# Kernel tuning notes

Measured on AMD Instinct MI355X. Metric: run time of the kernel, lower is better.

Reference implementation:

```python
import jax, jax.numpy as jnp
import numpy as np

N = 50000
E = 800000
C_IN, C_HID, C_OUT = 512, 128, 2
HEADS2 = 3
NEG_SLOPE = 0.2


def gat_conv(x, src, dst, W, att_src, att_dst, bias, heads, ch, concat):
    """PyG GATConv (eval mode) on pre-augmented (self-loop included) edge lists.
    x: [N, F_in], W: [F_in, heads*ch], att_*: [heads, ch], bias: [heads*ch] or [ch].
    """
    n = x.shape[0]
    h = (x @ W).reshape(n, heads, ch)                 # [N, H, C]
    a_src = (h * att_src).sum(-1)                     # [N, H]
    a_dst = (h * att_dst).sum(-1)                     # [N, H]
    e = jax.nn.leaky_relu(a_src[src] + a_dst[dst], NEG_SLOPE)  # [E', H]
    # segment softmax over edges sharing a destination node
    m = jax.ops.segment_max(e, dst, num_segments=n)
    m = jnp.where(jnp.isfinite(m), m, 0.0)
    ex = jnp.exp(e - m[dst])
    denom = jax.ops.segment_sum(ex, dst, num_segments=n)
    alpha = ex / (denom[dst] + 1e-16)                 # [E', H]
    out = jax.ops.segment_sum(h[src] * alpha[:, :, None], dst, num_segments=n)  # [N, H, C]
    out = out.reshape(n, heads * ch) if concat else out.mean(axis=1)
    return out + bias


def setup_inputs() -> dict:
    key = jax.random.key(0)
    ks = jax.random.split(key, 12)
    x = jax.random.normal(ks[0], (N, C_IN), dtype=jnp.float32)
    edge_index = jax.random.randint(ks[1], (2, E), 0, N, dtype=jnp.int64)
    s1 = 1.0 / np.sqrt(C_IN)
    s2 = 1.0 / np.sqrt(C_HID)
    return {
        "x": x,
        "edge_index": edge_index,
        "W1": jax.random.normal(ks[2], (C_IN, C_HID), dtype=jnp.float32) * s1,
        "att_src1": jax.random.normal(ks[3], (1, C_HID), dtype=jnp.float32) * s2,
        "att_dst1": jax.random.normal(ks[4], (1, C_HID), dtype=jnp.float32) * s2,
        "bias1": jnp.zeros((C_HID,), dtype=jnp.float32),
        "W2": jax.random.normal(ks[5], (C_HID, HEADS2 * C_OUT), dtype=jnp.float32) * s2,
        "att_src2": jax.random.normal(ks[6], (HEADS2, C_OUT), dtype=jnp.float32) * 0.5,
        "att_dst2": jax.random.normal(ks[7], (HEADS2, C_OUT), dtype=jnp.float32) * 0.5,
        "bias2": jnp.zeros((C_OUT,), dtype=jnp.float32),
    }


def reference(x, edge_index, W1, att_src1, att_dst1, bias1, W2, att_src2, att_dst2, bias2):
    n = x.shape[0]
    loop = jnp.arange(n, dtype=edge_index.dtype)
    src = jnp.concatenate([edge_index[0], loop])      # PyG add_self_loops=True
    dst = jnp.concatenate([edge_index[1], loop])
    h = gat_conv(x, src, dst, W1, att_src1, att_dst1, bias1, 1, C_HID, True)
    h = jax.nn.relu(h)                                # Dropout is identity in eval
    out = gat_conv(h, src, dst, W2, att_src2, att_dst2, bias2, HEADS2, C_OUT, False)
    return out
```

## Files before the change

### kernel.cpp

```cpp
#include <hip/hip_runtime.h>

#define N_NODES 50000
#define N_EDGES 800000
#define E_TOT   850000
#define C_IN    512
#define C_HID   128
#define NEG     0.2f

typedef _Float16 f16x8 __attribute__((ext_vector_type(8)));
typedef __attribute__((ext_vector_type(4))) float f32x4;

__device__ __forceinline__ float leaky(float x) { return x > 0.f ? x : NEG * x; }

union U32H2 { unsigned u; _Float16 h[2]; float f; };
union BFrag { uint4 u; f16x8 h; };

__device__ __forceinline__ unsigned short f2h(float f) {
  U32H2 c; c.h[0] = (_Float16)f; return (unsigned short)(c.u & 0xffff);
}

__device__ __forceinline__ unsigned pk2h(float a, float b) {
  union { __fp16 v __attribute__((ext_vector_type(2))); unsigned u; } c;
  c.v = __builtin_amdgcn_cvt_pkrtz(a, b);
  return c.u;
}

__device__ __forceinline__ float row_reduce_add(float v) {
  union { float f; int i; } a, b;
  a.f = v;
  b.i = __builtin_amdgcn_update_dpp(0, a.i, 0xB1, 0xF, 0xF, true);  a.f += b.f;
  b.i = __builtin_amdgcn_update_dpp(0, a.i, 0x4E, 0xF, 0xF, true);  a.f += b.f;
  b.i = __builtin_amdgcn_update_dpp(0, a.i, 0x124, 0xF, 0xF, true); a.f += b.f;
  b.i = __builtin_amdgcn_update_dpp(0, a.i, 0x128, 0xF, 0xF, true); a.f += b.f;
  return a.f;
}

__global__ __launch_bounds__(256) void setup_kernel(
    const float* __restrict__ W1, const float* __restrict__ as1,
    const float* __restrict__ ad1, const int* __restrict__ ei,
    unsigned short* __restrict__ Wswz, float* __restrict__ v1s, float* __restrict__ v1d,
    int* __restrict__ deg, int* __restrict__ rnk) {
  const int b = blockIdx.x;
  if (b < 32) {
    int t = b * 256 + threadIdx.x;
    int c = t >> 6, kc = t & 63;
    if (c >= C_HID) return;
    int kblk = kc >> 2, q = kc & 3;
    int ct = c >> 4, l15 = c & 15;
    int lane = q * 16 + l15;
    unsigned short hb[8], lb[8];
#pragma unroll
    for (int i = 0; i < 8; i++) {
      float w = W1[(size_t)(kc * 8 + i) * C_HID + c];
      _Float16 hi = (_Float16)w;
      _Float16 lo = (_Float16)(w - (float)hi);
      U32H2 ch; ch.h[0] = hi;
      U32H2 cl; cl.h[0] = lo;
      hb[i] = (unsigned short)(ch.u & 0xffff);
      lb[i] = (unsigned short)(cl.u & 0xffff);
    }
    size_t chunk0 = ((size_t)(kblk * 8 + ct) * 2) * 512;
    *(uint4*)&Wswz[chunk0 + (size_t)lane * 8]       = *(uint4*)hb;
    *(uint4*)&Wswz[chunk0 + 512 + (size_t)lane * 8] = *(uint4*)lb;
  } else if (b < 160) {
    const int wv = threadIdx.x >> 6, lane = threadIdx.x & 63;
    const int k = (b - 32) * 4 + wv;
    if (k >= C_IN) return;
    float2 w = *(const float2*)(W1 + (size_t)k * C_HID + 2 * lane);
    float2 a = *(const float2*)(as1 + 2 * lane);
    float2 d = *(const float2*)(ad1 + 2 * lane);
    float s = w.x * a.x + w.y * a.y;
    float t = w.x * d.x + w.y * d.y;
#pragma unroll
    for (int m = 32; m >= 1; m >>= 1) {
      s += __shfl_xor(s, m, 64);
      t += __shfl_xor(t, m, 64);
    }
    if (lane == 0) { v1s[k] = s; v1d[k] = t; }
  } else {
    int e = (b - 160) * 256 + threadIdx.x;
    if (e < N_EDGES) rnk[e] = atomicAdd(&deg[ei[N_EDGES + e]], 1);
  }
}

__global__ __launch_bounds__(256) void lin1_kernel(const float* __restrict__ x,
    const unsigned short* __restrict__ Wswz,
    const float* __restrict__ v1s, const float* __restrict__ v1d,
    unsigned short* __restrict__ h1u, float* __restrict__ a_src, float* __restrict__ a_dst,
    const int* __restrict__ deg, int* __restrict__ rowptr) {
  __shared__ __attribute__((aligned(16))) unsigned short As[2][64][40];
  __shared__ int wsum[4];

  if (blockIdx.x == 0) {
    const int tid = threadIdx.x, lane = tid & 63, wv = tid >> 6;
    int carry = 0;
    for (int base = 0; base < N_NODES; base += 8192) {
      int i0 = base + tid * 32;
      int v[32];
      if (i0 + 32 <= N_NODES) {
#pragma unroll
        for (int k = 0; k < 8; k++) {
          int4 t4 = *(const int4*)(deg + i0 + 4 * k);
          v[4 * k]     = t4.x + 1; v[4 * k + 1] = t4.y + 1;
          v[4 * k + 2] = t4.z + 1; v[4 * k + 3] = t4.w + 1;
        }
      } else {
#pragma unroll
        for (int k = 0; k < 32; k++) v[k] = (i0 + k < N_NODES) ? deg[i0 + k] + 1 : 0;
      }
      int tsum = 0;
#pragma unroll
      for (int k = 0; k < 32; k++) tsum += v[k];
      int sc = tsum;
#pragma unroll
      for (int off = 1; off < 64; off <<= 1) {
        int t = __shfl_up(sc, off, 64);
        if (lane >= off) sc += t;
      }
      if (lane == 63) wsum[wv] = sc;
      __syncthreads();
      if (tid < 4) {
        int s = wsum[tid];
#pragma unroll
        for (int off = 1; off < 4; off <<= 1) {
          int t = __shfl_up(s, off, 64);
          if (tid >= off) s += t;
        }
        wsum[tid] = s;
      }
      __syncthreads();
      int run = carry + (wv ? wsum[wv - 1] : 0) + sc - tsum;
      if (i0 + 32 <= N_NODES) {
#pragma unroll
        for (int k = 0; k < 8; k++) {
          int4 w4;
          w4.x = run; run += v[4 * k];
          w4.y = run; run += v[4 * k + 1];
          w4.z = run; run += v[4 * k + 2];
          w4.w = run; run += v[4 * k + 3];
          *(int4*)(rowptr + i0 + 4 * k) = w4;
        }
      } else {
#pragma unroll
        for (int k = 0; k < 32; k++) {
          if (i0 + k < N_NODES) rowptr[i0 + k] = run;
          run += v[k];
        }
      }
      carry += wsum[3];
      __syncthreads();
    }
    if (tid == 0) rowptr[N_NODES] = carry;
    return;
  }

  const int tid  = threadIdx.x;
  const int lane = tid & 63, wv = tid >> 6;
  const int m0   = (blockIdx.x - 1) * 64;

  const int arow = tid >> 2, kseg = (tid & 3) * 8;
  int grow = m0 + arow;
  if (grow >= N_NODES) grow = N_NODES - 1;
  const float* xrow = x + (size_t)grow * C_IN + kseg;

  f32x4 acc[4][2];
#pragma unroll
  for (int rt = 0; rt < 4; rt++) { acc[rt][0] = (f32x4)0.f; acc[rt][1] = (f32x4)0.f; }
  float ps = 0.f, pd = 0.f;

  const int q = lane >> 4, l15 = lane & 15;

  float4 xa = *(const float4*)(xrow);
  float4 xb = *(const float4*)(xrow + 4);

#pragma unroll
  for (int kblk = 0; kblk < 16; kblk++) {
    const int k0 = kblk * 32;
    const int buf = kblk & 1;
    float4 vsa = *(const float4*)(v1s + k0 + kseg);
    float4 vsb = *(const float4*)(v1s + k0 + kseg + 4);
    float4 vda = *(const float4*)(v1d + k0 + kseg);
    float4 vdb = *(const float4*)(v1d + k0 + kseg + 4);
    ps += xa.x * vsa.x + xa.y * vsa.y + xa.z * vsa.z + xa.w * vsa.w
        + xb.x * vsb.x + xb.y * vsb.y + xb.z * vsb.z + xb.w * vsb.w;
    pd += xa.x * vda.x + xa.y * vda.y + xa.z * vda.z + xa.w * vda.w
        + xb.x * vdb.x + xb.y * vdb.y + xb.z * vdb.z + xb.w * vdb.w;
    *(uint4*)&As[buf][arow][kseg] = make_uint4(pk2h(xa.x, xa.y), pk2h(xa.z, xa.w),
                                               pk2h(xb.x, xb.y), pk2h(xb.z, xb.w));
    __syncthreads();
    if (kblk < 15) {
      xa = *(const float4*)(xrow + k0 + 32);
      xb = *(const float4*)(xrow + k0 + 36);
    }

    const unsigned short* bp = Wswz + ((size_t)(kblk * 8 + wv * 2) * 2) * 512 + (size_t)lane * 8;
    BFrag b00, b01, b10, b11;
    b00.u = *(const uint4*)(bp);
    b01.u = *(const uint4*)(bp + 512);
    b10.u = *(const uint4*)(bp + 1024);
    b11.u = *(const uint4*)(bp + 1536);

#pragma unroll
    for (int rt = 0; rt < 4; rt++) {
      f16x8 af = *(const f16x8*)&As[buf][rt * 16 + l15][q * 8];
      acc[rt][0] = __builtin_amdgcn_mfma_f32_16x16x32_f16(af, b00.h, acc[rt][0], 0, 0, 0);
      acc[rt][0] = __builtin_amdgcn_mfma_f32_16x16x32_f16(af, b01.h, acc[rt][0], 0, 0, 0);
      acc[rt][1] = __builtin_amdgcn_mfma_f32_16x16x32_f16(af, b10.h, acc[rt][1], 0, 0, 0);
      acc[rt][1] = __builtin_amdgcn_mfma_f32_16x16x32_f16(af, b11.h, acc[rt][1], 0, 0, 0);
    }
  }

  ps += __shfl_xor(ps, 1, 64); ps += __shfl_xor(ps, 2, 64);
  pd += __shfl_xor(pd, 1, 64); pd += __shfl_xor(pd, 2, 64);
  if ((tid & 3) == 0) {
    int row = m0 + arow;
    if (row < N_NODES) { a_src[row] = ps; a_dst[row] = pd; }
  }

#pragma unroll
  for (int rt = 0; rt < 4; rt++) {
    int rbase = m0 + rt * 16 + q * 4;
#pragma unroll
    for (int ct = 0; ct < 2; ct++) {
      int col = wv * 32 + ct * 16 + l15;
#pragma unroll
      for (int ri = 0; ri < 4; ri++) {
        int row = rbase + ri;
        if (row < N_NODES)
          h1u[(size_t)row * C_HID + col] = f2h(acc[rt][ct][ri]);
      }
    }
  }
}

__global__ void bucket_kernel(const int* __restrict__ ei, const int* __restrict__ rnk,
                              const int* __restrict__ rowptr,
                              const float* __restrict__ a_src, const float* __restrict__ a_dst,
                              int2* __restrict__ esw) {
  int e = blockIdx.x * blockDim.x + threadIdx.x;
  if (e >= E_TOT) return;
  int src, slot;
  if (e < N_EDGES) {
    src = ei[e];
    int dst = ei[N_EDGES + e];
    slot = rowptr[dst] + rnk[e];
    U32H2 c; c.f = __expf(leaky(a_src[src] + a_dst[dst]));
    esw[slot] = make_int2(src, (int)c.u);
  } else {
    int n = e - N_EDGES;
    slot = rowptr[n + 1] - 1;
    U32H2 c; c.f = __expf(leaky(a_src[n] + a_dst[n]));
    esw[slot] = make_int2(n, (int)c.u);
  }
}

__global__ __launch_bounds__(256) void agg1_kernel(const unsigned short* __restrict__ h1u,
    const int2* __restrict__ esw, const int* __restrict__ rowptr,
    const float* __restrict__ bias1, const float* __restrict__ W2,
    const float* __restrict__ as2w, const float* __restrict__ ad2w,
    float* __restrict__ hs2) {
  const int wv = threadIdx.x >> 6, lane = threadIdx.x & 63;
  const int r = lane & 15;
  const int n = blockIdx.x * 16 + wv * 4 + (lane >> 4);
  const int start = rowptr[n], end = rowptr[n + 1];

  const unsigned short* hbase = h1u + r * 8;

  float acc[8] = {0, 0, 0, 0, 0, 0, 0, 0};
  float wsum = 0.f;
  for (int base = start; base < end; base += 8) {
    const int cnt = end - base;
    int2 rec[8];
#pragma unroll
    for (int j = 0; j < 8; j++)
      rec[j] = esw[j < cnt ? base + j : base];
    uint4 g[8];
#pragma unroll
    for (int j = 0; j < 8; j++)
      g[j] = *(const uint4*)(hbase + (size_t)rec[j].x * C_HID);
#pragma unroll
    for (int j = 0; j < 8; j++) {
      U32H2 cw; cw.u = (unsigned)rec[j].y;
      const float W = (j < cnt) ? cw.f : 0.f;
      wsum += W;
      U32H2 c0, c1, c2, c3;
      c0.u = g[j].x; c1.u = g[j].y; c2.u = g[j].z; c3.u = g[j].w;
      acc[0] = fmaf(W, (float)c0.h[0], acc[0]); acc[1] = fmaf(W, (float)c0.h[1], acc[1]);
      acc[2] = fmaf(W, (float)c1.h[0], acc[2]); acc[3] = fmaf(W, (float)c1.h[1], acc[3]);
      acc[4] = fmaf(W, (float)c2.h[0], acc[4]); acc[5] = fmaf(W, (float)c2.h[1], acc[5]);
      acc[6] = fmaf(W, (float)c3.h[0], acc[6]); acc[7] = fmaf(W, (float)c3.h[1], acc[7]);
    }
  }

  const float inv = 1.f / wsum;

  float4 ba = *(const float4*)(bias1 + r * 8);
  float4 bb = *(const float4*)(bias1 + r * 8 + 4);
  float u[8] = {fmaxf(acc[0] * inv + ba.x, 0.f), fmaxf(acc[1] * inv + ba.y, 0.f),
                fmaxf(acc[2] * inv + ba.z, 0.f), fmaxf(acc[3] * inv + ba.w, 0.f),
                fmaxf(acc[4] * inv + bb.x, 0.f), fmaxf(acc[5] * inv + bb.y, 0.f),
                fmaxf(acc[6] * inv + bb.z, 0.f), fmaxf(acc[7] * inv + bb.w, 0.f)};
  float p[6] = {0, 0, 0, 0, 0, 0};
#pragma unroll
  for (int j = 0; j < 8; j++) {
    const float* w2r = W2 + (size_t)(r * 8 + j) * 6;
#pragma unroll
    for (int o = 0; o < 6; o++) p[o] = fmaf(u[j], w2r[o], p[o]);
  }
#pragma unroll
  for (int o = 0; o < 6; o++) p[o] = row_reduce_add(p[o]);

  if (r == 0) {
    float as0 = p[0] * as2w[0] + p[1] * as2w[1];
    float as1 = p[2] * as2w[2] + p[3] * as2w[3];
    float as2_ = p[4] * as2w[4] + p[5] * as2w[5];
    float ad0 = p[0] * ad2w[0] + p[1] * ad2w[1];
    float ad1 = p[2] * ad2w[2] + p[3] * ad2w[3];
    float ad2_ = p[4] * ad2w[4] + p[5] * ad2w[5];
    float* dst = hs2 + (size_t)n * 12;
    *(float4*)(dst)     = make_float4(p[0], p[1], p[2], p[3]);
    *(float4*)(dst + 4) = make_float4(p[4], p[5], as0, as1);
    *(float4*)(dst + 8) = make_float4(as2_, ad0, ad1, ad2_);
  }
}

__global__ __launch_bounds__(256) void agg2_kernel(const float* __restrict__ hs2,
    const int* __restrict__ rowptr, const int2* __restrict__ esw,
    const float* __restrict__ bias2, float* __restrict__ out) {
  const int wv = threadIdx.x >> 6, lane = threadIdx.x & 63;
  const int q = lane >> 4, r = lane & 15;
  const int n = blockIdx.x * 16 + wv * 4 + q;
  if (n >= N_NODES) return;
  const int start = rowptr[n], end = rowptr[n + 1];
  float4 own = *(const float4*)(hs2 + (size_t)n * 12 + 8);
  const float ad0 = own.y, ad1 = own.z, ad2 = own.w;

  float d0 = 0.f, d1 = 0.f, d2 = 0.f;
  float a0 = 0.f, a1 = 0.f, a2 = 0.f, a3 = 0.f, a4 = 0.f, a5 = 0.f;
  for (int j = start + r; j < end; j += 16) {
    int s = esw[j].x;
    const float* rec = hs2 + (size_t)s * 12;
    float4 A = *(const float4*)(rec);
    float4 B = *(const float4*)(rec + 4);
    float  C = rec[8];
    float e0 = __expf(leaky(B.z + ad0));
    float e1 = __expf(leaky(B.w + ad1));
    float e2 = __expf(leaky(C + ad2));
    d0 += e0; d1 += e1; d2 += e2;
    a0 += e0 * A.x; a1 += e0 * A.y;
    a2 += e1 * A.z; a3 += e1 * A.w;
    a4 += e2 * B.x; a5 += e2 * B.y;
  }
  d0 = row_reduce_add(d0); d1 = row_reduce_add(d1); d2 = row_reduce_add(d2);
  a0 = row_reduce_add(a0); a1 = row_reduce_add(a1); a2 = row_reduce_add(a2);
  a3 = row_reduce_add(a3); a4 = row_reduce_add(a4); a5 = row_reduce_add(a5);
  if (r == 0) {
    float o0 = (a0 / d0 + a2 / d1 + a4 / d2) * (1.f / 3.f) + bias2[0];
    float o1 = (a1 / d0 + a3 / d1 + a5 / d2) * (1.f / 3.f) + bias2[1];
    *(float2*)(out + (size_t)n * 2) = make_float2(o0, o1);
  }
}

extern "C" void kernel_launch(void* const* d_in, const int* in_sizes, int n_in,
                              void* d_out, int out_size, void* d_ws, size_t ws_size,
                              hipStream_t stream) {
  const float* x        = (const float*)d_in[0];
  const int*   ei       = (const int*)d_in[1];
  const float* W1       = (const float*)d_in[2];
  const float* att_src1 = (const float*)d_in[3];
  const float* att_dst1 = (const float*)d_in[4];
  const float* bias1    = (const float*)d_in[5];
  const float* W2       = (const float*)d_in[6];
  const float* att_src2 = (const float*)d_in[7];
  const float* att_dst2 = (const float*)d_in[8];
  const float* bias2    = (const float*)d_in[9];
  float* out = (float*)d_out;

  char* w = (char*)d_ws;
  auto alloc = [&](size_t bytes) {
    char* p = w;
    w += (bytes + 255) & ~(size_t)255;
    return p;
  };
  unsigned short* h1u    = (unsigned short*)alloc((size_t)N_NODES * C_HID * 2);
  unsigned short* Wswz   = (unsigned short*)alloc((size_t)C_IN * C_HID * 2 * 2);
  float*          v1s    = (float*)alloc((size_t)C_IN * 4);
  float*          v1d    = (float*)alloc((size_t)C_IN * 4);
  float*          a_src1 = (float*)alloc((size_t)N_NODES * 4);
  float*          a_dst1 = (float*)alloc((size_t)N_NODES * 4);
  int*            deg    = (int*)alloc((size_t)N_NODES * 4);
  int*            rowptr = (int*)alloc((size_t)(N_NODES + 4) * 4);
  int*            rnk    = (int*)alloc((size_t)N_EDGES * 4);
  int2*           esw    = (int2*)alloc((size_t)E_TOT * 8);
  float*          hs2    = (float*)alloc((size_t)N_NODES * 12 * 4);

  (void)hipMemsetAsync(deg, 0, (size_t)N_NODES * 4, stream);

  setup_kernel<<<160 + (N_EDGES + 255) / 256, 256, 0, stream>>>(
      W1, att_src1, att_dst1, ei, Wswz, v1s, v1d, deg, rnk);
  lin1_kernel<<<(N_NODES + 63) / 64 + 1, 256, 0, stream>>>(x, Wswz, v1s, v1d,
                                                           h1u, a_src1, a_dst1,
                                                           deg, rowptr);
  bucket_kernel<<<(E_TOT + 255) / 256, 256, 0, stream>>>(ei, rnk, rowptr,
                                                         a_src1, a_dst1, esw);
  agg1_kernel<<<N_NODES / 16, 256, 0, stream>>>(h1u, esw, rowptr, bias1, W2,
                                                att_src2, att_dst2, hs2);
  agg2_kernel<<<(N_NODES + 15) / 16, 256, 0, stream>>>(hs2, rowptr, esw, bias2, out);
}
```

Measured before the change: 293.2 us.

## Load MFMA A-fragments directly from global, dropping LDS staging and barriers

The lin1 GEMM is restructured so each wave loads its A-operand rows of x straight into registers in MFMA fragment layout, instead of staging through shared memory with a per-k-block __syncthreads. Waves are re-tiled as 2x2 (32 rows x 64 cols each) rather than 4 column slices covering all 64 rows. This removes LDS writes, reads and block barriers, but each x row is now loaded by two waves (wc=0/1) and each wave reads more W fragments per k-block. The attention dot products are redistributed to match the new row ownership.

```diff
diff --git a/kernel.cpp b/kernel.cpp
--- a/kernel.cpp
+++ b/kernel.cpp
@@ -14,6 +14,7 @@
 
 union U32H2 { unsigned u; _Float16 h[2]; float f; };
 union BFrag { uint4 u; f16x8 h; };
+union AFrag { unsigned u[4]; f16x8 h; };
 
 __device__ __forceinline__ unsigned short f2h(float f) {
   U32H2 c; c.h[0] = (_Float16)f; return (unsigned short)(c.u & 0xffff);
@@ -88,7 +89,6 @@
     const float* __restrict__ v1s, const float* __restrict__ v1d,
     unsigned short* __restrict__ h1u, float* __restrict__ a_src, float* __restrict__ a_dst,
     const int* __restrict__ deg, int* __restrict__ rowptr) {
-  __shared__ __attribute__((aligned(16))) unsigned short As[2][64][40];
   __shared__ int wsum[4];
 
   if (blockIdx.x == 0) {
@@ -156,73 +156,88 @@
 
   const int tid  = threadIdx.x;
   const int lane = tid & 63, wv = tid >> 6;
-  const int m0   = (blockIdx.x - 1) * 64;
-
-  const int arow = tid >> 2, kseg = (tid & 3) * 8;
-  int grow = m0 + arow;
-  if (grow >= N_NODES) grow = N_NODES - 1;
-  const float* xrow = x + (size_t)grow * C_IN + kseg;
-
-  f32x4 acc[4][2];
-#pragma unroll
-  for (int rt = 0; rt < 4; rt++) { acc[rt][0] = (f32x4)0.f; acc[rt][1] = (f32x4)0.f; }
-  float ps = 0.f, pd = 0.f;
-
-  const int q = lane >> 4, l15 = lane & 15;
-
-  float4 xa = *(const float4*)(xrow);
-  float4 xb = *(const float4*)(xrow + 4);
+  const int wr = wv >> 1, wc = wv & 1;
+  const int q = lane >> 4, r15 = lane & 15;
+  const int m0 = (blockIdx.x - 1) * 64;
+
+  const int row0 = m0 + wr * 32 + r15;
+  const int row1 = row0 + 16;
+  const int lr0 = min(row0, N_NODES - 1);
+  const int lr1 = min(row1, N_NODES - 1);
+  const float* xr0 = x + (size_t)lr0 * C_IN + q * 8;
+  const float* xr1 = x + (size_t)lr1 * C_IN + q * 8;
+  const float* vsp = v1s + q * 8;
+  const float* vdp = v1d + q * 8;
+
+  f32x4 acc[2][4];
+#pragma unroll
+  for (int rt = 0; rt < 2; rt++)
+#pragma unroll
+    for (int ct = 0; ct < 4; ct++) acc[rt][ct] = (f32x4)0.f;
+  float ps0 = 0.f, pd0 = 0.f, ps1 = 0.f, pd1 = 0.f;
+
+  float4 a0a = *(const float4*)(xr0);
+  float4 a0b = *(const float4*)(xr0 + 4);
+  float4 a1a = *(const float4*)(xr1);
+  float4 a1b = *(const float4*)(xr1 + 4);
 
 #pragma unroll
   for (int kblk = 0; kblk < 16; kblk++) {
     const int k0 = kblk * 32;
-    const int buf = kblk & 1;
-    float4 vsa = *(const float4*)(v1s + k0 + kseg);
-    float4 vsb = *(const float4*)(v1s + k0 + kseg + 4);
-    float4 vda = *(const float4*)(v1d + k0 + kseg);
-    float4 vdb = *(const float4*)(v1d + k0 + kseg + 4);
-    ps += xa.x * vsa.x + xa.y * vsa.y + xa.z * vsa.z + xa.w * vsa.w
-        + xb.x * vsb.x + xb.y * vsb.y + xb.z * vsb.z + xb.w * vsb.w;
-    pd += xa.x * vda.x + xa.y * vda.y + xa.z * vda.z + xa.w * vda.w
-        + xb.x * vdb.x + xb.y * vdb.y + xb.z * vdb.z + xb.w * vdb.w;
-    *(uint4*)&As[buf][arow][kseg] = make_uint4(pk2h(xa.x, xa.y), pk2h(xa.z, xa.w),
-                                               pk2h(xb.x, xb.y), pk2h(xb.z, xb.w));
-    __syncthreads();
+    float4 vsa = *(const float4*)(vsp + k0);
+    float4 vsb = *(const float4*)(vsp + k0 + 4);
+    float4 vda = *(const float4*)(vdp + k0);
+    float4 vdb = *(const float4*)(vdp + k0 + 4);
+    ps0 += a0a.x * vsa.x + a0a.y * vsa.y + a0a.z * vsa.z + a0a.w * vsa.w
+         + a0b.x * vsb.x + a0b.y * vsb.y + a0b.z * vsb.z + a0b.w * vsb.w;
+    pd0 += a0a.x * vda.x + a0a.y * vda.y + a0a.z * vda.z + a0a.w * vda.w
+         + a0b.x * vdb.x + a0b.y * vdb.y + a0b.z * vdb.z + a0b.w * vdb.w;
+    ps1 += a1a.x * vsa.x + a1a.y * vsa.y + a1a.z * vsa.z + a1a.w * vsa.w
+         + a1b.x * vsb.x + a1b.y * vsb.y + a1b.z * vsb.z + a1b.w * vsb.w;
+    pd1 += a1a.x * vda.x + a1a.y * vda.y + a1a.z * vda.z + a1a.w * vda.w
+         + a1b.x * vdb.x + a1b.y * vdb.y + a1b.z * vdb.z + a1b.w * vdb.w;
+
+    AFrag af0, af1;
+    af0.u[0] = pk2h(a0a.x, a0a.y); af0.u[1] = pk2h(a0a.z, a0a.w);
+    af0.u[2] = pk2h(a0b.x, a0b.y); af0.u[3] = pk2h(a0b.z, a0b.w);
+    af1.u[0] = pk2h(a1a.x, a1a.y); af1.u[1] = pk2h(a1a.z, a1a.w);
+    af1.u[2] = pk2h(a1b.x, a1b.y); af1.u[3] = pk2h(a1b.z, a1b.w);
+
     if (kblk < 15) {
-      xa = *(const float4*)(xrow + k0 + 32);
-      xb = *(const float4*)(xrow + k0 + 36);
-    }
-
-    const unsigned short* bp = Wswz + ((size_t)(kblk * 8 + wv * 2) * 2) * 512 + (size_t)lane * 8;
-    BFrag b00, b01, b10, b11;
-    b00.u = *(const uint4*)(bp);
-    b01.u = *(const uint4*)(bp + 512);
-    b10.u = *(const uint4*)(bp + 1024);
-    b11.u = *(const uint4*)(bp + 1536);
-
-#pragma unroll
-    for (int rt = 0; rt < 4; rt++) {
-      f16x8 af = *(const f16x8*)&As[buf][rt * 16 + l15][q * 8];
-      acc[rt][0] = __builtin_amdgcn_mfma_f32_16x16x32_f16(af, b00.h, acc[rt][0], 0, 0, 0);
-      acc[rt][0] = __builtin_amdgcn_mfma_f32_16x16x32_f16(af, b01.h, acc[rt][0], 0, 0, 0);
-      acc[rt][1] = __builtin_amdgcn_mfma_f32_16x16x32_f16(af, b10.h, acc[rt][1], 0, 0, 0);
-      acc[rt][1] = __builtin_amdgcn_mfma_f32_16x16x32_f16(af, b11.h, acc[rt][1], 0, 0, 0);
-    }
-  }
-
-  ps += __shfl_xor(ps, 1, 64); ps += __shfl_xor(ps, 2, 64);
-  pd += __shfl_xor(pd, 1, 64); pd += __shfl_xor(pd, 2, 64);
-  if ((tid & 3) == 0) {
-    int row = m0 + arow;
-    if (row < N_NODES) { a_src[row] = ps; a_dst[row] = pd; }
-  }
-
-#pragma unroll
-  for (int rt = 0; rt < 4; rt++) {
-    int rbase = m0 + rt * 16 + q * 4;
-#pragma unroll
-    for (int ct = 0; ct < 2; ct++) {
-      int col = wv * 32 + ct * 16 + l15;
+      a0a = *(const float4*)(xr0 + k0 + 32);
+      a0b = *(const float4*)(xr0 + k0 + 36);
+      a1a = *(const float4*)(xr1 + k0 + 32);
+      a1b = *(const float4*)(xr1 + k0 + 36);
+    }
+
+    const unsigned short* bp = Wswz + (size_t)(kblk * 8 + wc * 4) * 1024 + (size_t)lane * 8;
+#pragma unroll
+    for (int ct = 0; ct < 4; ct++) {
+      BFrag bh, bl;
+      bh.u = *(const uint4*)(bp + ct * 1024);
+      bl.u = *(const uint4*)(bp + ct * 1024 + 512);
+      acc[0][ct] = __builtin_amdgcn_mfma_f32_16x16x32_f16(af0.h, bh.h, acc[0][ct], 0, 0, 0);
+      acc[0][ct] = __builtin_amdgcn_mfma_f32_16x16x32_f16(af0.h, bl.h, acc[0][ct], 0, 0, 0);
+      acc[1][ct] = __builtin_amdgcn_mfma_f32_16x16x32_f16(af1.h, bh.h, acc[1][ct], 0, 0, 0);
+      acc[1][ct] = __builtin_amdgcn_mfma_f32_16x16x32_f16(af1.h, bl.h, acc[1][ct], 0, 0, 0);
+    }
+  }
+
+  ps0 += __shfl_xor(ps0, 16, 64); ps0 += __shfl_xor(ps0, 32, 64);
+  pd0 += __shfl_xor(pd0, 16, 64); pd0 += __shfl_xor(pd0, 32, 64);
+  ps1 += __shfl_xor(ps1, 16, 64); ps1 += __shfl_xor(ps1, 32, 64);
+  pd1 += __shfl_xor(pd1, 16, 64); pd1 += __shfl_xor(pd1, 32, 64);
+  if (q == 0) {
+    if (row0 < N_NODES) { a_src[row0] = ps0; a_dst[row0] = pd0; }
+    if (row1 < N_NODES) { a_src[row1] = ps1; a_dst[row1] = pd1; }
+  }
+
+#pragma unroll
+  for (int rt = 0; rt < 2; rt++) {
+    int rbase = m0 + wr * 32 + rt * 16 + q * 4;
+#pragma unroll
+    for (int ct = 0; ct < 4; ct++) {
+      int col = wc * 64 + ct * 16 + r15;
 #pragma unroll
       for (int ri = 0; ri < 4; ri++) {
         int row = rbase + ri;
```

Result: slower. 308.5 us (+5.2%).

## Deepen lin1 K-blocking with bigger register prefetch and prefetch agg1 edge records

Applied to the files above, without the earlier changes.

lin1 now stages four 32-wide K slices per barrier (128-wide K blocks) with a 4x larger shared buffer and prefetched x registers, so it hits a barrier four times instead of sixteen. It also sets launch_bounds occupancy to 3. agg1 software-pipelines the edge-record loads by fetching the next 8 records while the current gathers run. The costs are higher register and shared-memory use, which may lower occupancy, and possible spills under the launch bound.

```diff
diff --git a/kernel.cpp b/kernel.cpp
--- a/kernel.cpp
+++ b/kernel.cpp
@@ -83,12 +83,12 @@
   }
 }
 
-__global__ __launch_bounds__(256) void lin1_kernel(const float* __restrict__ x,
+__global__ __launch_bounds__(256, 3) void lin1_kernel(const float* __restrict__ x,
     const unsigned short* __restrict__ Wswz,
     const float* __restrict__ v1s, const float* __restrict__ v1d,
     unsigned short* __restrict__ h1u, float* __restrict__ a_src, float* __restrict__ a_dst,
     const int* __restrict__ deg, int* __restrict__ rowptr) {
-  __shared__ __attribute__((aligned(16))) unsigned short As[2][64][40];
+  __shared__ __attribute__((aligned(16))) unsigned short As[2][4][64][40];
   __shared__ int wsum[4];
 
   if (blockIdx.x == 0) {
@@ -170,43 +170,65 @@
 
   const int q = lane >> 4, l15 = lane & 15;
 
-  float4 xa = *(const float4*)(xrow);
-  float4 xb = *(const float4*)(xrow + 4);
-
-#pragma unroll
-  for (int kblk = 0; kblk < 16; kblk++) {
-    const int k0 = kblk * 32;
-    const int buf = kblk & 1;
-    float4 vsa = *(const float4*)(v1s + k0 + kseg);
-    float4 vsb = *(const float4*)(v1s + k0 + kseg + 4);
-    float4 vda = *(const float4*)(v1d + k0 + kseg);
-    float4 vdb = *(const float4*)(v1d + k0 + kseg + 4);
-    ps += xa.x * vsa.x + xa.y * vsa.y + xa.z * vsa.z + xa.w * vsa.w
-        + xb.x * vsb.x + xb.y * vsb.y + xb.z * vsb.z + xb.w * vsb.w;
-    pd += xa.x * vda.x + xa.y * vda.y + xa.z * vda.z + xa.w * vda.w
-        + xb.x * vdb.x + xb.y * vdb.y + xb.z * vdb.z + xb.w * vdb.w;
-    *(uint4*)&As[buf][arow][kseg] = make_uint4(pk2h(xa.x, xa.y), pk2h(xa.z, xa.w),
-                                               pk2h(xb.x, xb.y), pk2h(xb.z, xb.w));
+  float4 xp[4][2];
+#pragma unroll
+  for (int s = 0; s < 4; s++) {
+    xp[s][0] = *(const float4*)(xrow + s * 32);
+    xp[s][1] = *(const float4*)(xrow + s * 32 + 4);
+  }
+
+#pragma unroll
+  for (int kb = 0; kb < 4; kb++) {
+    const int k0 = kb * 128;
+    const int buf = kb & 1;
+#pragma unroll
+    for (int s = 0; s < 4; s++) {
+      float4 vsa = *(const float4*)(v1s + k0 + s * 32 + kseg);
+      float4 vsb = *(const float4*)(v1s + k0 + s * 32 + kseg + 4);
+      float4 vda = *(const float4*)(v1d + k0 + s * 32 + kseg);
+      float4 vdb = *(const float4*)(v1d + k0 + s * 32 + kseg + 4);
+      ps += xp[s][0].x * vsa.x + xp[s][0].y * vsa.y + xp[s][0].z * vsa.z + xp[s][0].w * vsa.w
+          + xp[s][1].x * vsb.x + xp[s][1].y * vsb.y + xp[s][1].z * vsb.z + xp[s][1].w * vsb.w;
+      pd += xp[s][0].x * vda.x + xp[s][0].y * vda.y + xp[s][0].z * vda.z + xp[s][0].w * vda.w
+          + xp[s][1].x * vdb.x + xp[s][1].y * vdb.y + xp[s][1].z * vdb.z + xp[s][1].w * vdb.w;
+      *(uint4*)&As[buf][s][arow][kseg] =
+          make_uint4(pk2h(xp[s][0].x, xp[s][0].y), pk2h(xp[s][0].z, xp[s][0].w),
+                     pk2h(xp[s][1].x, xp[s][1].y), pk2h(xp[s][1].z, xp[s][1].w));
+    }
     __syncthreads();
-    if (kblk < 15) {
-      xa = *(const float4*)(xrow + k0 + 32);
-      xb = *(const float4*)(xrow + k0 + 36);
-    }
-
-    const unsigned short* bp = Wswz + ((size_t)(kblk * 8 + wv * 2) * 2) * 512 + (size_t)lane * 8;
-    BFrag b00, b01, b10, b11;
-    b00.u = *(const uint4*)(bp);
-    b01.u = *(const uint4*)(bp + 512);
-    b10.u = *(const uint4*)(bp + 1024);
-    b11.u = *(const uint4*)(bp + 1536);
-
-#pragma unroll
-    for (int rt = 0; rt < 4; rt++) {
-      f16x8 af = *(const f16x8*)&As[buf][rt * 16 + l15][q * 8];
-      acc[rt][0] = __builtin_amdgcn_mfma_f32_16x16x32_f16(af, b00.h, acc[rt][0], 0, 0, 0);
-      acc[rt][0] = __builtin_amdgcn_mfma_f32_16x16x32_f16(af, b01.h, acc[rt][0], 0, 0, 0);
-      acc[rt][1] = __builtin_amdgcn_mfma_f32_16x16x32_f16(af, b10.h, acc[rt][1], 0, 0, 0);
-      acc[rt][1] = __builtin_amdgcn_mfma_f32_16x16x32_f16(af, b11.h, acc[rt][1], 0, 0, 0);
+    if (kb < 3) {
+#pragma unroll
+      for (int s = 0; s < 4; s++) {
+        xp[s][0] = *(const float4*)(xrow + k0 + 128 + s * 32);
+        xp[s][1] = *(const float4*)(xrow + k0 + 128 + s * 32 + 4);
+      }
+    }
+
+#pragma unroll
+    for (int sp = 0; sp < 2; sp++) {
+      BFrag bf[2][4];
+#pragma unroll
+      for (int s = 0; s < 2; s++) {
+        const int sub = sp * 2 + s;
+        const unsigned short* bp =
+            Wswz + ((size_t)((kb * 4 + sub) * 8 + wv * 2) * 2) * 512 + (size_t)lane * 8;
+        bf[s][0].u = *(const uint4*)(bp);
+        bf[s][1].u = *(const uint4*)(bp + 512);
+        bf[s][2].u = *(const uint4*)(bp + 1024);
+        bf[s][3].u = *(const uint4*)(bp + 1536);
+      }
+#pragma unroll
+      for (int rt = 0; rt < 4; rt++) {
+#pragma unroll
+        for (int s = 0; s < 2; s++) {
+          const int sub = sp * 2 + s;
+          f16x8 af = *(const f16x8*)&As[buf][sub][rt * 16 + l15][q * 8];
+          acc[rt][0] = __builtin_amdgcn_mfma_f32_16x16x32_f16(af, bf[s][0].h, acc[rt][0], 0, 0, 0);
+          acc[rt][0] = __builtin_amdgcn_mfma_f32_16x16x32_f16(af, bf[s][1].h, acc[rt][0], 0, 0, 0);
+          acc[rt][1] = __builtin_amdgcn_mfma_f32_16x16x32_f16(af, bf[s][2].h, acc[rt][1], 0, 0, 0);
+          acc[rt][1] = __builtin_amdgcn_mfma_f32_16x16x32_f16(af, bf[s][3].h, acc[rt][1], 0, 0, 0);
+        }
+      }
     }
   }
 
@@ -268,12 +290,23 @@
 
   float acc[8] = {0, 0, 0, 0, 0, 0, 0, 0};
   float wsum = 0.f;
-  for (int base = start; base < end; base += 8) {
-    const int cnt = end - base;
-    int2 rec[8];
-#pragma unroll
-    for (int j = 0; j < 8; j++)
-      rec[j] = esw[j < cnt ? base + j : base];
+
+  int base = start;
+  int cnt = min(end - base, 8);
+  int2 rec[8];
+#pragma unroll
+  for (int j = 0; j < 8; j++) rec[j] = esw[j < cnt ? base + j : base];
+
+  while (true) {
+    const int nbase = base + 8;
+    const bool more = nbase < end;
+    int ncnt = 0;
+    int2 nrec[8];
+    if (more) {
+      ncnt = min(end - nbase, 8);
+#pragma unroll
+      for (int j = 0; j < 8; j++) nrec[j] = esw[j < ncnt ? nbase + j : nbase];
+    }
     uint4 g[8];
 #pragma unroll
     for (int j = 0; j < 8; j++)
@@ -290,6 +323,10 @@
       acc[4] = fmaf(W, (float)c2.h[0], acc[4]); acc[5] = fmaf(W, (float)c2.h[1], acc[5]);
       acc[6] = fmaf(W, (float)c3.h[0], acc[6]); acc[7] = fmaf(W, (float)c3.h[1], acc[7]);
     }
+    if (!more) break;
+    base = nbase; cnt = ncnt;
+#pragma unroll
+    for (int j = 0; j < 8; j++) rec[j] = nrec[j];
   }
 
   const float inv = 1.f / wsum;
```

Result: no change. 291.0 us, median of 2 (-0.7%).
